# Optimization experiments

Measured on AMD Instinct MI355X. Metric: run time of the kernel, lower is better.

Reference implementation:

```python
import jax, jax.numpy as jnp
import numpy as np

N_HEAD = 16


def setup_inputs() -> dict:
    key = jax.random.key(0)
    ks = jax.random.split(key, 6)
    B, T, C = 2, 2048, 1024
    hs = C // N_HEAD  # 64
    block_minus_1 = 2048  # block_size - 1
    x = jax.random.normal(ks[0], (B, T, C), dtype=jnp.float32)
    W1 = jax.random.normal(ks[1], (C, C), dtype=jnp.float32) * (1.0 / np.sqrt(C))
    b1 = jnp.zeros((C,), dtype=jnp.float32)
    # original init: uniform(-1e-3, 1e-3)
    w2 = jax.random.uniform(ks[2], (hs, block_minus_1), dtype=jnp.float32, minval=-1e-3, maxval=1e-3)
    b2 = jnp.zeros((block_minus_1,), dtype=jnp.float32)
    Wv = jax.random.normal(ks[3], (C, C), dtype=jnp.float32) * (1.0 / np.sqrt(C))
    bv = jnp.zeros((C,), dtype=jnp.float32)
    Wp = jax.random.normal(ks[4], (C, C), dtype=jnp.float32) * (1.0 / np.sqrt(C))
    bp = jnp.zeros((C,), dtype=jnp.float32)
    return {"x": x, "W1": W1, "b1": b1, "w2": w2, "b2": b2,
            "Wv": Wv, "bv": bv, "Wp": Wp, "bp": bp}


def reference(x, W1, b1, w2, b2, Wv, bv, Wp, bp):
    B, T, C = x.shape
    hs = C // N_HEAD
    r = jax.nn.relu(x @ W1.T + b1).reshape(B, T, N_HEAD, hs).transpose(0, 2, 1, 3)
    # synthesizer scores: (B, nh, T, T) = relu_out @ w2[:, :T] + b2[:T]
    att = jnp.einsum('bhtd,dj->bhtj', r, w2[:, :T]) + b2[:T]
    causal = jnp.tril(jnp.ones((T, T), dtype=bool))
    att = jnp.where(causal[None, None], att, jnp.float32(-1e10))
    att = jax.nn.softmax(att, axis=-1)  # attn_drop = 0 (eval)
    v = (x @ Wv.T + bv).reshape(B, T, N_HEAD, hs).transpose(0, 2, 1, 3)
    y = jnp.einsum('bhtj,bhjd->bhtd', att, v)
    y = y.transpose(0, 2, 1, 3).reshape(B, T, C)
    return y @ Wp.T + bp  # resid_drop = 0 (eval)
```

## Files before the change

kernel.cpp:

```cpp
#include <hip/hip_runtime.h>

typedef __bf16 bf16x8 __attribute__((ext_vector_type(8)));
typedef float f32x4 __attribute__((ext_vector_type(4)));

__device__ __forceinline__ unsigned short f2bf(float f) {
  union { float f; unsigned u; } v; v.f = f;
  unsigned u = v.u;
  return (unsigned short)((u + 0x7fffu + ((u >> 16) & 1u)) >> 16);
}
__device__ __forceinline__ unsigned short f2bf_fast(float f) {
  union { float f; unsigned u; } v; v.f = f;
  return (unsigned short)((v.u + 0x8000u) >> 16);
}
__device__ __forceinline__ void gload_lds16(const void* g, void* l) {
  __builtin_amdgcn_global_load_lds(
      (const __attribute__((address_space(1))) unsigned int*)g,
      (__attribute__((address_space(3))) unsigned int*)l, 16, 0, 0);
}
__device__ __forceinline__ void cvt4(const float* __restrict__ s,
                                     unsigned short* __restrict__ d, int u) {
  f32x4 v = ((const f32x4*)s)[u];
  union { unsigned short s[4]; unsigned long long u; } o;
  o.s[0] = f2bf(v[0]); o.s[1] = f2bf(v[1]); o.s[2] = f2bf(v[2]); o.s[3] = f2bf(v[3]);
  ((unsigned long long*)d)[u] = o.u;
}


__global__ void prep(const float* __restrict__ x, const float* __restrict__ W1,
                     const float* __restrict__ Wv, const float* __restrict__ Wp,
                     const float* __restrict__ w2, const float* __restrict__ b2,
                     unsigned short* __restrict__ xb, unsigned short* __restrict__ W1b,
                     unsigned short* __restrict__ Wvb, unsigned short* __restrict__ Wpb,
                     unsigned short* __restrict__ w2t, unsigned short* __restrict__ ebj) {
  int u = blockIdx.x * 256 + threadIdx.x;
  if (u < 1048576) { cvt4(x, xb, u); return; }
  u -= 1048576;
  if (u < 262144) { cvt4(W1, W1b, u); return; }
  u -= 262144;
  if (u < 262144) { cvt4(Wv, Wvb, u); return; }
  u -= 262144;
  if (u < 262144) { cvt4(Wp, Wpb, u); return; }
  u -= 262144;
  if (u < 32768) {
    int j = u >> 4, d4 = (u & 15) * 4;
    union { unsigned short s[4]; unsigned long long x; } o;
#pragma unroll
    for (int i = 0; i < 4; ++i) o.s[i] = f2bf(w2[(d4 + i) * 2048 + j]);
    ((unsigned long long*)w2t)[u] = o.x;
    return;
  }
  u -= 32768;
  union { unsigned short s[4]; unsigned long long x; } o;
#pragma unroll
  for (int i = 0; i < 4; ++i) o.s[i] = f2bf(__expf(b2[u * 4 + i]));
  ((unsigned long long*)ebj)[u] = o.x;
}

__global__ __launch_bounds__(256) void gemm_rv(
    const unsigned short* __restrict__ xb, const unsigned short* __restrict__ W1b,
    const unsigned short* __restrict__ Wvb, const float* __restrict__ b1,
    const float* __restrict__ bv, const float* __restrict__ b2,
    unsigned short* __restrict__ rb, unsigned short* __restrict__ vtb) {
  __shared__ unsigned short Xs[64 * 64];
  __shared__ unsigned short W1s[64 * 64];
  __shared__ unsigned short Wvs[64 * 64];
  const int tm = blockIdx.x * 64, n0 = blockIdx.y * 64;
  const int tid = threadIdx.x;
  const int wv = tid >> 6, ln = tid & 63;
  const int quad = ln >> 4, lq = ln & 15;
  const int rowL = ln >> 3;
  const int kc = (((ln & 7) ^ rowL) & 7) * 8;
  const int sx = lq & 7;
  const int ko0 = (quad ^ sx) * 8, ko1 = ((4 + quad) ^ sx) * 8;

  f32x4 accR[4], accV[4];
  const f32x4 zf = {0.f, 0.f, 0.f, 0.f};
#pragma unroll
  for (int j = 0; j < 4; ++j) { accR[j] = zf; accV[j] = zf; }

  for (int k0 = 0; k0 < 1024; k0 += 64) {
    __syncthreads();
#pragma unroll
    for (int l = 0; l < 2; ++l) {
      int row = l * 32 + wv * 8 + rowL;
      gload_lds16(xb + (tm + row) * 1024 + k0 + kc, &Xs[l * 2048 + wv * 512]);
      gload_lds16(W1b + (n0 + row) * 1024 + k0 + kc, &W1s[l * 2048 + wv * 512]);
      gload_lds16(Wvb + (n0 + row) * 1024 + k0 + kc, &Wvs[l * 2048 + wv * 512]);
    }
    __syncthreads();
#pragma unroll
    for (int kk = 0; kk < 2; ++kk) {
      const int ko = kk ? ko1 : ko0;
      bf16x8 xa  = *(const bf16x8*)&Xs[(wv * 16 + lq) * 64 + ko];
      bf16x8 wva = *(const bf16x8*)&Wvs[(wv * 16 + lq) * 64 + ko];
#pragma unroll
      for (int ni = 0; ni < 4; ++ni) {
        bf16x8 w1f = *(const bf16x8*)&W1s[(ni * 16 + lq) * 64 + ko];
        accR[ni] = __builtin_amdgcn_mfma_f32_16x16x32_bf16(xa, w1f, accR[ni], 0, 0, 0);
      }
#pragma unroll
      for (int nj = 0; nj < 4; ++nj) {
        bf16x8 xbf = *(const bf16x8*)&Xs[(nj * 16 + lq) * 64 + ko];
        accV[nj] = __builtin_amdgcn_mfma_f32_16x16x32_bf16(wva, xbf, accV[nj], 0, 0, 0);
      }
    }
  }
#pragma unroll
  for (int ni = 0; ni < 4; ++ni) {
    int col = n0 + ni * 16 + lq;
    float bc = b1[col];
#pragma unroll
    for (int rg = 0; rg < 4; ++rg) {
      int row = tm + wv * 16 + quad * 4 + rg;
      float v = accR[ni][rg] + bc;
      rb[row * 1024 + col] = f2bf(v > 0.f ? v : 0.f);
    }
  }
  float bvv[4];
#pragma unroll
  for (int rg = 0; rg < 4; ++rg) bvv[rg] = bv[n0 + wv * 16 + quad * 4 + rg];
#pragma unroll
  for (int nj = 0; nj < 4; ++nj) {
    int tok = tm + nj * 16 + lq;
    float eb = __expf(b2[tok & 2047]);
#pragma unroll
    for (int rg = 0; rg < 4; ++rg) {
      int ch = n0 + wv * 16 + quad * 4 + rg;
      vtb[ch * 4096 + tok] = f2bf((accV[nj][rg] + bvv[rg]) * eb);
    }
  }
}

__global__ __launch_bounds__(256) void gemm_p(
    const unsigned short* __restrict__ A, const unsigned short* __restrict__ Bt,
    const float* __restrict__ bias, float* __restrict__ C) {
  __shared__ unsigned short As[64 * 128];
  __shared__ unsigned short Bs[64 * 128];
  const int tid = threadIdx.x;
  const int wv = tid >> 6, ln = tid & 63;
  const int quad = ln >> 4, lq = ln & 15;
  const int tileM = blockIdx.y * 64, tileN = blockIdx.x * 64;
  const int srow = ln >> 4, pos = ln & 15;

  f32x4 acc[4];
  const f32x4 zf = {0.f, 0.f, 0.f, 0.f};
#pragma unroll
  for (int j = 0; j < 4; ++j) acc[j] = zf;

  int kof[4];
#pragma unroll
  for (int kk = 0; kk < 4; ++kk) {
    int c = kk * 4 + quad;
    kof[kk] = (((c & 8) | ((c & 7) ^ (lq & 7)))) * 8;
  }

  for (int k0 = 0; k0 < 1024; k0 += 128) {
    __syncthreads();
#pragma unroll
    for (int l = 0; l < 4; ++l) {
      int row = l * 16 + wv * 4 + srow;
      int cs = (pos & 8) | ((pos & 7) ^ (row & 7));
      gload_lds16(A + (tileM + row) * 1024 + k0 + cs * 8, &As[(l * 16 + wv * 4) * 128]);
      gload_lds16(Bt + (tileN + row) * 1024 + k0 + cs * 8, &Bs[(l * 16 + wv * 4) * 128]);
    }
    __syncthreads();
#pragma unroll
    for (int kk = 0; kk < 4; ++kk) {
      const int ko = kof[kk];
      bf16x8 af = *(const bf16x8*)&As[(wv * 16 + lq) * 128 + ko];
#pragma unroll
      for (int ni = 0; ni < 4; ++ni) {
        bf16x8 bfr = *(const bf16x8*)&Bs[(ni * 16 + lq) * 128 + ko];
        acc[ni] = __builtin_amdgcn_mfma_f32_16x16x32_bf16(af, bfr, acc[ni], 0, 0, 0);
      }
    }
  }
#pragma unroll
  for (int ni = 0; ni < 4; ++ni) {
    int col = tileN + ni * 16 + lq;
#pragma unroll
    for (int rg = 0; rg < 4; ++rg) {
      int row = tileM + wv * 16 + quad * 4 + rg;
      C[row * 1024 + col] = acc[ni][rg] + bias[col];
    }
  }
}

__global__ __launch_bounds__(256, 2) void attn(
    const unsigned short* __restrict__ r, const unsigned short* __restrict__ w2t,
    const unsigned short* __restrict__ vt, const unsigned short* __restrict__ ebj,
    unsigned short* __restrict__ y) {
  __shared__ unsigned short W2s[2][64 * 64];
  __shared__ unsigned short Vs[2][64 * 64];
  __shared__ unsigned short Ps[4][16 * 64];

  const int tid = threadIdx.x;
  const int wv = tid >> 6, ln = tid & 63;
  const int quad = ln >> 4, lq = ln & 15;
  const int bh = blockIdx.x, b = bh >> 4, h = bh & 15;
  const int q = blockIdx.y;
  const int p = (q < 8) ? q : 23 - q;
  const int ta = p, tb = 31 - p;
  const int t0a = ta * 64, t0b = tb * 64;
  const int rowL = ln >> 3;
  const int kc = (((ln & 7) ^ rowL) & 7) * 8;
  const int sx = lq & 7;
  const int ko0 = (quad ^ sx) * 8, ko1 = ((4 + quad) ^ sx) * 8;

  bf16x8 ra[2][2];
  {
    const unsigned short* base = r + (b * 2048 + wv * 16 + lq) * 1024 + h * 64 + quad * 8;
    ra[0][0] = *(const bf16x8*)(base + t0a * 1024);
    ra[0][1] = *(const bf16x8*)(base + t0a * 1024 + 32);
    ra[1][0] = *(const bf16x8*)(base + t0b * 1024);
    ra[1][1] = *(const bf16x8*)(base + t0b * 1024 + 32);
  }

  f32x4 accY[2][4];
  f32x4 accL[2];
  const f32x4 zf = {0.f, 0.f, 0.f, 0.f};
#pragma unroll
  for (int s = 0; s < 2; ++s) {
    accL[s] = zf;
#pragma unroll
    for (int nd = 0; nd < 4; ++nd) accY[s][nd] = zf;
  }

  auto stage = [&](int jt, int bi) {
    int j0 = jt * 64;
#pragma unroll
    for (int l = 0; l < 2; ++l) {
      int row = l * 32 + wv * 8 + rowL;
      gload_lds16(w2t + (j0 + row) * 64 + kc, &W2s[bi][l * 2048 + wv * 512]);
      gload_lds16(vt + (h * 64 + row) * 4096 + b * 2048 + j0 + kc,
                  &Vs[bi][l * 2048 + wv * 512]);
    }
  };

#define TILE(S, T0, TT)                                                         \
    {                                                                           \
      f32x4 sv[4] = {zf, zf, zf, zf};                                           \
      _Pragma("unroll") for (int ni = 0; ni < 4; ++ni) {                        \
        sv[ni] = __builtin_amdgcn_mfma_f32_16x16x32_bf16(ra[S][0], w2f0[ni], sv[ni], 0, 0, 0); \
        sv[ni] = __builtin_amdgcn_mfma_f32_16x16x32_bf16(ra[S][1], w2f1[ni], sv[ni], 0, 0, 0); \
      }                                                                         \
      const bool diag = (jt == (TT));                                           \
      _Pragma("unroll") for (int ni = 0; ni < 4; ++ni) {                        \
        int j = j0 + ni * 16 + lq;                                              \
        _Pragma("unroll") for (int rg = 0; rg < 4; ++rg) {                      \
          float pe = __expf(sv[ni][rg]);                                        \
          if (diag) {                                                           \
            int t = (T0) + wv * 16 + quad * 4 + rg;                             \
            pe = (j <= t) ? pe : 0.f;                                           \
          }                                                                     \
          Ps[wv][(quad * 4 + rg) * 64 +                                         \
                 (((ni * 2 + (lq >> 3)) ^ ((quad * 4 + rg) & 7)) * 8) + (lq & 7)] = f2bf_fast(pe); \
        }                                                                       \
      }                                                                         \
      _Pragma("unroll") for (int kk = 0; kk < 2; ++kk) {                        \
        const int ko = kk ? ko1 : ko0;                                          \
        bf16x8 pa = *(const bf16x8*)&Ps[wv][lq * 64 + ko];                      \
        _Pragma("unroll") for (int nd = 0; nd < 4; ++nd) {                      \
          bf16x8 bb = *(const bf16x8*)&Vs[cb][(nd * 16 + lq) * 64 + ko];        \
          accY[S][nd] = __builtin_amdgcn_mfma_f32_16x16x32_bf16(pa, bb, accY[S][nd], 0, 0, 0); \
        }                                                                       \
        accL[S] = __builtin_amdgcn_mfma_f32_16x16x32_bf16(pa, kk ? eb1 : eb0, accL[S], 0, 0, 0); \
      }                                                                         \
    }

#define WRITEOUT(S, T0)                                                         \
    {                                                                           \
      float inv[4];                                                             \
      _Pragma("unroll") for (int rg = 0; rg < 4; ++rg)                          \
        inv[rg] = __builtin_amdgcn_rcpf(accL[S][rg]);                           \
      _Pragma("unroll") for (int nd = 0; nd < 4; ++nd)                          \
        _Pragma("unroll") for (int rg = 0; rg < 4; ++rg) {                      \
          int t = (T0) + wv * 16 + quad * 4 + rg;                               \
          y[(b * 2048 + t) * 1024 + h * 64 + nd * 16 + lq] =                    \
              f2bf(accY[S][nd][rg] * inv[rg]);                                  \
        }                                                                       \
    }

  stage(0, 0);
  for (int jt = 0; jt <= tb; ++jt) {
    const int cb = jt & 1;
    __syncthreads();
    if (jt < tb) stage(jt + 1, cb ^ 1);
    const int j0 = jt * 64;

    bf16x8 eb0 = *(const bf16x8*)&ebj[j0 + quad * 8];
    bf16x8 eb1 = *(const bf16x8*)&ebj[j0 + 32 + quad * 8];
    bf16x8 w2f0[4], w2f1[4];
#pragma unroll
    for (int ni = 0; ni < 4; ++ni) {
      w2f0[ni] = *(const bf16x8*)&W2s[cb][(ni * 16 + lq) * 64 + ko0];
      w2f1[ni] = *(const bf16x8*)&W2s[cb][(ni * 16 + lq) * 64 + ko1];
    }

    if (jt <= ta) TILE(0, t0a, ta);
    TILE(1, t0b, tb);
    if (jt == ta) WRITEOUT(0, t0a);
  }
  WRITEOUT(1, t0b);
#undef TILE
#undef WRITEOUT
}

extern "C" void kernel_launch(void* const* d_in, const int* in_sizes, int n_in,
                              void* d_out, int out_size, void* d_ws, size_t ws_size,
                              hipStream_t stream) {
  const float* x  = (const float*)d_in[0];
  const float* W1 = (const float*)d_in[1];
  const float* b1 = (const float*)d_in[2];
  const float* w2 = (const float*)d_in[3];
  const float* b2 = (const float*)d_in[4];
  const float* Wv = (const float*)d_in[5];
  const float* bv = (const float*)d_in[6];
  const float* Wp = (const float*)d_in[7];
  const float* bp = (const float*)d_in[8];

  unsigned short* ws  = (unsigned short*)d_ws;
  unsigned short* xb   = ws;
  unsigned short* W1b  = ws + 4194304;
  unsigned short* Wvb  = ws + 5242880;
  unsigned short* Wpb  = ws + 6291456;
  unsigned short* w2t  = ws + 7340032;
  unsigned short* rb   = ws + 7471104;
  unsigned short* vt   = ws + 11665408;
  unsigned short* yb   = ws + 15859712;
  unsigned short* ebjb = ws + 20054016;

  prep<<<7298, 256, 0, stream>>>(x, W1, Wv, Wp, w2, b2, xb, W1b, Wvb, Wpb, w2t, ebjb);
  gemm_rv<<<dim3(64, 16), 256, 0, stream>>>(xb, W1b, Wvb, b1, bv, b2, rb, vt);
  attn<<<dim3(32, 16), 256, 0, stream>>>(rb, w2t, vt, ebjb, yb);
  gemm_p<<<dim3(16, 64), 256, 0, stream>>>(yb, Wpb, bp, (float*)d_out);
}
```

Before: 170.7 us.

## Software-pipeline attention loop: overlap PV of previous tile with scores of next

Restructures the attention inner loop into a skewed software pipeline. Iteration jt runs the P·V MFMAs for tile jt-1 and then computes the scores and exp for tile jt, so the exp/LDS-store latency can overlap with matrix work. To support this, P gets a double buffer and V gets a triple buffer in LDS, and s_setprio raises wave priority around the MFMA bursts. The cost is more LDS per block, which may reduce occupancy, plus an extra loop iteration and more register pressure.

```diff
diff --git a/kernel.cpp b/kernel.cpp
--- a/kernel.cpp
+++ b/kernel.cpp
@@ -191,8 +191,8 @@
     const unsigned short* __restrict__ vt, const unsigned short* __restrict__ ebj,
     unsigned short* __restrict__ y) {
   __shared__ unsigned short W2s[2][64 * 64];
-  __shared__ unsigned short Vs[2][64 * 64];
-  __shared__ unsigned short Ps[4][16 * 64];
+  __shared__ unsigned short Vs[3][64 * 64];
+  __shared__ unsigned short Ps[2][4][16 * 64];
 
   const int tid = threadIdx.x;
   const int wv = tid >> 6, ln = tid & 63;
@@ -226,45 +226,46 @@
     for (int nd = 0; nd < 4; ++nd) accY[s][nd] = zf;
   }
 
-  auto stage = [&](int jt, int bi) {
+  auto stage = [&](int jt) {
     int j0 = jt * 64;
+    unsigned short* W2d = &W2s[jt & 1][0];
+    unsigned short* Vd = &Vs[jt % 3][0];
 #pragma unroll
     for (int l = 0; l < 2; ++l) {
       int row = l * 32 + wv * 8 + rowL;
-      gload_lds16(w2t + (j0 + row) * 64 + kc, &W2s[bi][l * 2048 + wv * 512]);
+      gload_lds16(w2t + (j0 + row) * 64 + kc, W2d + l * 2048 + wv * 512);
       gload_lds16(vt + (h * 64 + row) * 4096 + b * 2048 + j0 + kc,
-                  &Vs[bi][l * 2048 + wv * 512]);
+                  Vd + l * 2048 + wv * 512);
     }
   };
 
-#define TILE(S, T0, TT)                                                         \
+#define PV(S, VB, EB0, EB1)                                                     \
     {                                                                           \
-      f32x4 sv[4] = {zf, zf, zf, zf};                                           \
-      _Pragma("unroll") for (int ni = 0; ni < 4; ++ni) {                        \
-        sv[ni] = __builtin_amdgcn_mfma_f32_16x16x32_bf16(ra[S][0], w2f0[ni], sv[ni], 0, 0, 0); \
-        sv[ni] = __builtin_amdgcn_mfma_f32_16x16x32_bf16(ra[S][1], w2f1[ni], sv[ni], 0, 0, 0); \
+      _Pragma("unroll") for (int kk = 0; kk < 2; ++kk) {                        \
+        const int ko = kk ? ko1 : ko0;                                          \
+        bf16x8 pa = *(const bf16x8*)&Ps[S][wv][lq * 64 + ko];                   \
+        _Pragma("unroll") for (int nd = 0; nd < 4; ++nd) {                      \
+          bf16x8 bb = *(const bf16x8*)&Vs[VB][(nd * 16 + lq) * 64 + ko];        \
+          accY[S][nd] = __builtin_amdgcn_mfma_f32_16x16x32_bf16(pa, bb, accY[S][nd], 0, 0, 0); \
+        }                                                                       \
+        accL[S] = __builtin_amdgcn_mfma_f32_16x16x32_bf16(pa, kk ? (EB1) : (EB0), accL[S], 0, 0, 0); \
       }                                                                         \
+    }
+
+#define EXPSTORE(S, SV, T0, TT)                                                 \
+    {                                                                           \
       const bool diag = (jt == (TT));                                           \
       _Pragma("unroll") for (int ni = 0; ni < 4; ++ni) {                        \
         int j = j0 + ni * 16 + lq;                                              \
         _Pragma("unroll") for (int rg = 0; rg < 4; ++rg) {                      \
-          float pe = __expf(sv[ni][rg]);                                        \
+          float pe = __expf(SV[ni][rg]);                                        \
           if (diag) {                                                           \
             int t = (T0) + wv * 16 + quad * 4 + rg;                             \
             pe = (j <= t) ? pe : 0.f;                                           \
           }                                                                     \
-          Ps[wv][(quad * 4 + rg) * 64 +                                         \
-                 (((ni * 2 + (lq >> 3)) ^ ((quad * 4 + rg) & 7)) * 8) + (lq & 7)] = f2bf_fast(pe); \
+          Ps[S][wv][(quad * 4 + rg) * 64 +                                      \
+                    (((ni * 2 + (lq >> 3)) ^ ((quad * 4 + rg) & 7)) * 8) + (lq & 7)] = f2bf_fast(pe); \
         }                                                                       \
-      }                                                                         \
-      _Pragma("unroll") for (int kk = 0; kk < 2; ++kk) {                        \
-        const int ko = kk ? ko1 : ko0;                                          \
-        bf16x8 pa = *(const bf16x8*)&Ps[wv][lq * 64 + ko];                      \
-        _Pragma("unroll") for (int nd = 0; nd < 4; ++nd) {                      \
-          bf16x8 bb = *(const bf16x8*)&Vs[cb][(nd * 16 + lq) * 64 + ko];        \
-          accY[S][nd] = __builtin_amdgcn_mfma_f32_16x16x32_bf16(pa, bb, accY[S][nd], 0, 0, 0); \
-        }                                                                       \
-        accL[S] = __builtin_amdgcn_mfma_f32_16x16x32_bf16(pa, kk ? eb1 : eb0, accL[S], 0, 0, 0); \
       }                                                                         \
     }
 
@@ -281,28 +282,62 @@
         }                                                                       \
     }
 
-  stage(0, 0);
-  for (int jt = 0; jt <= tb; ++jt) {
-    const int cb = jt & 1;
-    __syncthreads();
-    if (jt < tb) stage(jt + 1, cb ^ 1);
-    const int j0 = jt * 64;
-
-    bf16x8 eb0 = *(const bf16x8*)&ebj[j0 + quad * 8];
-    bf16x8 eb1 = *(const bf16x8*)&ebj[j0 + 32 + quad * 8];
-    bf16x8 w2f0[4], w2f1[4];
-#pragma unroll
-    for (int ni = 0; ni < 4; ++ni) {
-      w2f0[ni] = *(const bf16x8*)&W2s[cb][(ni * 16 + lq) * 64 + ko0];
-      w2f1[ni] = *(const bf16x8*)&W2s[cb][(ni * 16 + lq) * 64 + ko1];
-    }
-
-    if (jt <= ta) TILE(0, t0a, ta);
-    TILE(1, t0b, tb);
-    if (jt == ta) WRITEOUT(0, t0a);
-  }
-  WRITEOUT(1, t0b);
-#undef TILE
+  stage(0);
+
+  for (int jt = 0; jt <= tb + 1; ++jt) {
+    const int pj = jt - 1;
+    const bool doS = (jt <= tb);
+    const bool doSa = (jt <= ta);
+
+    if (doS) {
+      __syncthreads();
+      if (jt < tb) stage(jt + 1);
+    }
+
+    if (pj >= 0) {
+      const int vb = pj % 3;
+      const int j0p = pj * 64;
+      bf16x8 eb0 = *(const bf16x8*)&ebj[j0p + quad * 8];
+      bf16x8 eb1 = *(const bf16x8*)&ebj[j0p + 32 + quad * 8];
+      __builtin_amdgcn_s_setprio(1);
+      if (pj <= ta) PV(0, vb, eb0, eb1);
+      PV(1, vb, eb0, eb1);
+      __builtin_amdgcn_s_setprio(0);
+    }
+
+    if (doS) {
+      const int wb = jt & 1;
+      const int j0 = jt * 64;
+      bf16x8 w2f0[4], w2f1[4];
+#pragma unroll
+      for (int ni = 0; ni < 4; ++ni) {
+        w2f0[ni] = *(const bf16x8*)&W2s[wb][(ni * 16 + lq) * 64 + ko0];
+        w2f1[ni] = *(const bf16x8*)&W2s[wb][(ni * 16 + lq) * 64 + ko1];
+      }
+      f32x4 sv0[4], sv1[4];
+      __builtin_amdgcn_s_setprio(1);
+      if (doSa) {
+#pragma unroll
+        for (int ni = 0; ni < 4; ++ni) {
+          sv0[ni] = __builtin_amdgcn_mfma_f32_16x16x32_bf16(ra[0][0], w2f0[ni], zf, 0, 0, 0);
+          sv0[ni] = __builtin_amdgcn_mfma_f32_16x16x32_bf16(ra[0][1], w2f1[ni], sv0[ni], 0, 0, 0);
+        }
+      }
+#pragma unroll
+      for (int ni = 0; ni < 4; ++ni) {
+        sv1[ni] = __builtin_amdgcn_mfma_f32_16x16x32_bf16(ra[1][0], w2f0[ni], zf, 0, 0, 0);
+        sv1[ni] = __builtin_amdgcn_mfma_f32_16x16x32_bf16(ra[1][1], w2f1[ni], sv1[ni], 0, 0, 0);
+      }
+      __builtin_amdgcn_s_setprio(0);
+      if (doSa) EXPSTORE(0, sv0, t0a, ta);
+      EXPSTORE(1, sv1, t0b, tb);
+    }
+
+    if (pj == ta) WRITEOUT(0, t0a);
+    if (pj == tb) WRITEOUT(1, t0b);
+  }
+#undef PV
+#undef EXPSTORE
 #undef WRITEOUT
 }
 
```

After: 178.8 us. +4.8%, slower.

## Keep softmax probabilities in registers via transposed MFMA and permlane swaps

Applied to the files above, without the earlier changes.

Computes the score tile transposed (swapping the MFMA operands) so each lane holds values for a single query row. It then packs the probabilities to bf16 with v_cvt_pk_bf16_f32 and rearranges them into A-operand layout with permlane32/permlane16 swaps, instead of round-tripping through the per-wave Ps LDS buffer. This removes the LDS stores and loads and frees shared memory. The risk is that the operand and K-index ordering must exactly match the swizzled V layout (ko0/ko1). Rounding also changes from round-half-up to the hardware's packed conversion.

```diff
diff --git a/kernel.cpp b/kernel.cpp
--- a/kernel.cpp
+++ b/kernel.cpp
@@ -8,14 +8,15 @@
   unsigned u = v.u;
   return (unsigned short)((u + 0x7fffu + ((u >> 16) & 1u)) >> 16);
 }
-__device__ __forceinline__ unsigned short f2bf_fast(float f) {
-  union { float f; unsigned u; } v; v.f = f;
-  return (unsigned short)((v.u + 0x8000u) >> 16);
-}
 __device__ __forceinline__ void gload_lds16(const void* g, void* l) {
   __builtin_amdgcn_global_load_lds(
       (const __attribute__((address_space(1))) unsigned int*)g,
       (__attribute__((address_space(3))) unsigned int*)l, 16, 0, 0);
+}
+__device__ __forceinline__ unsigned cvtpk(float lo, float hi) {
+  unsigned r;
+  asm("v_cvt_pk_bf16_f32 %0, %1, %2" : "=v"(r) : "v"(lo), "v"(hi));
+  return r;
 }
 __device__ __forceinline__ void cvt4(const float* __restrict__ s,
                                      unsigned short* __restrict__ d, int u) {
@@ -192,7 +193,6 @@
     unsigned short* __restrict__ y) {
   __shared__ unsigned short W2s[2][64 * 64];
   __shared__ unsigned short Vs[2][64 * 64];
-  __shared__ unsigned short Ps[4][16 * 64];
 
   const int tid = threadIdx.x;
   const int wv = tid >> 6, ln = tid & 63;
@@ -239,33 +239,47 @@
 
 #define TILE(S, T0, TT)                                                         \
     {                                                                           \
-      f32x4 sv[4] = {zf, zf, zf, zf};                                           \
+      f32x4 sv[4];                                                              \
       _Pragma("unroll") for (int ni = 0; ni < 4; ++ni) {                        \
-        sv[ni] = __builtin_amdgcn_mfma_f32_16x16x32_bf16(ra[S][0], w2f0[ni], sv[ni], 0, 0, 0); \
-        sv[ni] = __builtin_amdgcn_mfma_f32_16x16x32_bf16(ra[S][1], w2f1[ni], sv[ni], 0, 0, 0); \
+        sv[ni] = __builtin_amdgcn_mfma_f32_16x16x32_bf16(w2f0[ni], ra[S][0], zf, 0, 0, 0); \
+        sv[ni] = __builtin_amdgcn_mfma_f32_16x16x32_bf16(w2f1[ni], ra[S][1], sv[ni], 0, 0, 0); \
       }                                                                         \
       const bool diag = (jt == (TT));                                           \
-      _Pragma("unroll") for (int ni = 0; ni < 4; ++ni) {                        \
-        int j = j0 + ni * 16 + lq;                                              \
+      const int tl = (T0) + wv * 16 + lq;                                       \
+      _Pragma("unroll") for (int ni = 0; ni < 4; ++ni)                          \
         _Pragma("unroll") for (int rg = 0; rg < 4; ++rg) {                      \
           float pe = __expf(sv[ni][rg]);                                        \
           if (diag) {                                                           \
-            int t = (T0) + wv * 16 + quad * 4 + rg;                             \
-            pe = (j <= t) ? pe : 0.f;                                           \
+            int j = j0 + ni * 16 + quad * 4 + rg;                               \
+            pe = (j <= tl) ? pe : 0.f;                                          \
           }                                                                     \
-          Ps[wv][(quad * 4 + rg) * 64 +                                         \
-                 (((ni * 2 + (lq >> 3)) ^ ((quad * 4 + rg) & 7)) * 8) + (lq & 7)] = f2bf_fast(pe); \
+          sv[ni][rg] = pe;                                                      \
         }                                                                       \
+      bf16x8 pa0, pa1;                                                          \
+      {                                                                         \
+        union { unsigned u[4]; bf16x8 v; } k0u, k1u;                            \
+        _Pragma("unroll") for (int pr = 0; pr < 2; ++pr) {                      \
+          unsigned a0 = cvtpk(sv[0][2 * pr], sv[0][2 * pr + 1]);                \
+          unsigned b0 = cvtpk(sv[1][2 * pr], sv[1][2 * pr + 1]);                \
+          asm("v_permlane32_swap_b32 %0, %1" : "+v"(a0), "+v"(b0));             \
+          asm("v_permlane16_swap_b32 %0, %1" : "+v"(a0), "+v"(b0));             \
+          k0u.u[pr] = a0; k0u.u[2 + pr] = b0;                                   \
+          unsigned a1 = cvtpk(sv[2][2 * pr], sv[2][2 * pr + 1]);                \
+          unsigned b1 = cvtpk(sv[3][2 * pr], sv[3][2 * pr + 1]);                \
+          asm("v_permlane32_swap_b32 %0, %1" : "+v"(a1), "+v"(b1));             \
+          asm("v_permlane16_swap_b32 %0, %1" : "+v"(a1), "+v"(b1));             \
+          k1u.u[pr] = a1; k1u.u[2 + pr] = b1;                                   \
+        }                                                                       \
+        pa0 = k0u.v; pa1 = k1u.v;                                               \
       }                                                                         \
-      _Pragma("unroll") for (int kk = 0; kk < 2; ++kk) {                        \
-        const int ko = kk ? ko1 : ko0;                                          \
-        bf16x8 pa = *(const bf16x8*)&Ps[wv][lq * 64 + ko];                      \
-        _Pragma("unroll") for (int nd = 0; nd < 4; ++nd) {                      \
-          bf16x8 bb = *(const bf16x8*)&Vs[cb][(nd * 16 + lq) * 64 + ko];        \
-          accY[S][nd] = __builtin_amdgcn_mfma_f32_16x16x32_bf16(pa, bb, accY[S][nd], 0, 0, 0); \
-        }                                                                       \
-        accL[S] = __builtin_amdgcn_mfma_f32_16x16x32_bf16(pa, kk ? eb1 : eb0, accL[S], 0, 0, 0); \
+      _Pragma("unroll") for (int nd = 0; nd < 4; ++nd) {                        \
+        bf16x8 bb0 = *(const bf16x8*)&Vs[cb][(nd * 16 + lq) * 64 + ko0];        \
+        accY[S][nd] = __builtin_amdgcn_mfma_f32_16x16x32_bf16(pa0, bb0, accY[S][nd], 0, 0, 0); \
+        bf16x8 bb1 = *(const bf16x8*)&Vs[cb][(nd * 16 + lq) * 64 + ko1];        \
+        accY[S][nd] = __builtin_amdgcn_mfma_f32_16x16x32_bf16(pa1, bb1, accY[S][nd], 0, 0, 0); \
       }                                                                         \
+      accL[S] = __builtin_amdgcn_mfma_f32_16x16x32_bf16(pa0, eb0, accL[S], 0, 0, 0); \
+      accL[S] = __builtin_amdgcn_mfma_f32_16x16x32_bf16(pa1, eb1, accL[S], 0, 0, 0); \
     }
 
 #define WRITEOUT(S, T0)                                                         \
```

New measurement: 166.8 us. -2.3%, faster.
